# Optimization experiments

Hardware: AMD Instinct MI355X
Metric: run time of the kernel (lower is better)

Reference implementation:

```python
import jax, jax.numpy as jnp
import numpy as np

NB, H, C, HID, EMB = 4, 12, 1024, 768, 512
E, M, L, SPAN = 22, 4, 16, 32
TD, INTER = 20, 256
NN = E + E * M + L
NREL, NLAYERS = 3, 4

def _build_adj():
    # static relational adjacency: r0 entity<->its mentions, r1 mention<->co-entity mention, r2 mention<->link
    A = np.zeros((NREL, NN, NN), np.float32)
    for e in range(E):
        for m in range(M):
            mi = E + e * M + m
            A[0, e, mi] = A[0, mi, e] = 1.0
            for m2 in range(M):
                if m2 != m:
                    A[1, mi, E + e * M + m2] = 1.0
            li = E + E * M + ((e * M + m) % L)
            A[2, mi, li] = A[2, li, mi] = 1.0
    A = A / (A.sum(-1, keepdims=True) + 1e-5)
    return jnp.asarray(A)

_ADJ = _build_adj()
_TYPES = np.concatenate([np.zeros(E, np.int32), np.ones(E * M, np.int32), np.full(L, 2, np.int32)])

def _forward(sequence_output, attention, W_trans, b_trans, type_embed,
             rgcn_Wrel0, rgcn_Wself0, rgcn_Wrel, rgcn_Wself,
             fs_w1, fs_b1, fs_g1, fs_be1, fs_w2, fs_b2, fs_g2, fs_be2,
             fc_w1, fc_b1, fc_g1, fc_be1, fc_w2, fc_b2, fc_g2, fc_be2,
             cr_w1, cr_b1, cr_w2, cr_b2, cr_w3, cr_b3,
             mention_idx, link_start):
    n = sequence_output.shape[0]
    b = jnp.arange(n)[:, None, None]
    seq = sequence_output @ W_trans + b_trans            # [n,C,EMB] extractor_trans
    attq = attention.transpose(0, 2, 1, 3)               # [n,C,H,C] query-major
    # --- make_graph: mention / entity nodes (gather + logsumexp pooling) ---
    m_rep = seq[b, mention_idx]                          # [n,E,M,EMB]
    m_att = attq[b, mention_idx]                         # [n,E,M,H,C]
    e_rep = jax.nn.logsumexp(m_rep, axis=2)              # [n,E,EMB]
    e_att = m_att.mean(axis=2)                           # [n,E,H,C]
    # --- link nodes: attention-weighted span pooling ---
    idx = link_start[:, :, None] + jnp.arange(SPAN)      # [n,L,SPAN]
    span = seq[b, idx]                                   # [n,L,SPAN,EMB]
    att_rows = attq[b, idx]                              # [n,L,SPAN,H,C]
    col_idx = jnp.broadcast_to(idx[:, :, None, None, :], (n, L, SPAN, H, SPAN))
    block = jnp.take_along_axis(att_rows, col_idx, axis=4).mean(axis=3)  # [n,L,SPAN,SPAN]
    link_rep = jnp.einsum('nlst,nltd->nld', block, span) / SPAN          # [n,L,EMB]
    # --- node matrix + type embedding ---
    nodes = jnp.concatenate([e_rep, m_rep.reshape(n, E * M, EMB), link_rep], axis=1)
    tfeat = jnp.broadcast_to(type_embed[_TYPES][None], (n, NN, TD))
    h = jnp.concatenate([nodes, tfeat], axis=-1)         # [n,NN,EMB+TD]
    # --- RGCN ---
    def rgcn_layer(hh, Wrel, Wself):
        msg = jnp.einsum('rij,njd,rdo->nio', _ADJ, hh, Wrel)
        return jax.nn.relu(msg + hh @ Wself)
    h = rgcn_layer(h, rgcn_Wrel0, rgcn_Wself0)
    for l in range(NLAYERS - 1):
        h = rgcn_layer(h, rgcn_Wrel[l], rgcn_Wself[l])
    # --- relation_map: structure + attention-weighted context ---
    entity_stru = h[:, :E]                               # [n,E,EMB]
    ea = e_att.mean(axis=2)                              # [n,E,C]
    ea = ea / (ea.sum(-1, keepdims=True) + 1e-5)
    e_ctx = jnp.einsum('nec,ncd->ned', ea, seq)          # [n,E,EMB]
    ec = entity_stru + e_ctx
    fmap = (ec[:, :, None, :] * ec[:, None, :, :]).transpose(0, 3, 1, 2)  # [n,EMB,E,E]
    # --- SE fusion (fusion_s / fusion_c, BN in eval form) ---
    conv1x1 = lambda x, w, bb: jnp.einsum('nchw,oc->nohw', x, w) + bb[None, :, None, None]
    bn = lambda x, g, be: x * g[None, :, None, None] + be[None, :, None, None]
    s = bn(conv1x1(jax.nn.relu(bn(conv1x1(fmap, fs_w1, fs_b1), fs_g1, fs_be1)), fs_w2, fs_b2), fs_g2, fs_be2)
    pooled = fmap.mean(axis=(2, 3), keepdims=True)
    cb = bn(conv1x1(jax.nn.relu(bn(conv1x1(pooled, fc_w1, fc_b1), fc_g1, fc_be1)), fc_w2, fc_b2), fc_g2, fc_be2)
    fused = fmap * jax.nn.sigmoid(s + cb)
    # --- conv_reason 5x5 blocks ---
    dn = ('NCHW', 'OIHW', 'NCHW')
    conv = lambda x, w, bb: jax.lax.conv_general_dilated(x, w, (1, 1), 'SAME', dimension_numbers=dn) + bb[None, :, None, None]
    r = jax.nn.relu(conv(fused, cr_w1, cr_b1))
    r = jax.nn.relu(conv(r, cr_w2, cr_b2))
    return jax.nn.relu(conv(r, cr_w3, cr_b3))            # [n,EMB,E,E]

def setup_inputs():
    key = jax.random.key(0)
    ks = jax.random.split(key, 24)
    p = lambda k, sh: jax.random.normal(k, sh, jnp.float32) * 0.02
    z = lambda sh: jnp.zeros(sh, jnp.float32)
    o = lambda sh: jnp.ones(sh, jnp.float32)
    return {
        'sequence_output': jax.random.normal(ks[0], (NB, C, HID), jnp.float32),
        'attention': jax.random.uniform(ks[1], (NB, H, C, C), jnp.float32),
        'W_trans': p(ks[2], (HID, EMB)), 'b_trans': z((EMB,)),
        'type_embed': p(ks[3], (3, TD)),
        'rgcn_Wrel0': p(ks[4], (NREL, EMB + TD, EMB)), 'rgcn_Wself0': p(ks[5], (EMB + TD, EMB)),
        'rgcn_Wrel': p(ks[6], (NLAYERS - 1, NREL, EMB, EMB)), 'rgcn_Wself': p(ks[7], (NLAYERS - 1, EMB, EMB)),
        'fs_w1': p(ks[8], (INTER, EMB)), 'fs_b1': z((INTER,)), 'fs_g1': o((INTER,)), 'fs_be1': z((INTER,)),
        'fs_w2': p(ks[9], (EMB, INTER)), 'fs_b2': z((EMB,)), 'fs_g2': o((EMB,)), 'fs_be2': z((EMB,)),
        'fc_w1': p(ks[10], (INTER, EMB)), 'fc_b1': z((INTER,)), 'fc_g1': o((INTER,)), 'fc_be1': z((INTER,)),
        'fc_w2': p(ks[11], (EMB, INTER)), 'fc_b2': z((EMB,)), 'fc_g2': o((EMB,)), 'fc_be2': z((EMB,)),
        'cr_w1': p(ks[12], (INTER, EMB, 5, 5)), 'cr_b1': z((INTER,)),
        'cr_w2': p(ks[13], (INTER, INTER, 5, 5)), 'cr_b2': z((INTER,)),
        'cr_w3': p(ks[14], (EMB, INTER, 5, 5)), 'cr_b3': z((EMB,)),
        'mention_idx': jax.random.randint(ks[15], (NB, E, M), 0, C),
        'link_start': jnp.sort(jax.random.randint(ks[16], (NB, L), 0, C - SPAN), axis=-1),
    }

def reference(sequence_output, attention, W_trans, b_trans, type_embed,
              rgcn_Wrel0, rgcn_Wself0, rgcn_Wrel, rgcn_Wself,
              fs_w1, fs_b1, fs_g1, fs_be1, fs_w2, fs_b2, fs_g2, fs_be2,
              fc_w1, fc_b1, fc_g1, fc_be1, fc_w2, fc_b2, fc_g2, fc_be2,
              cr_w1, cr_b1, cr_w2, cr_b2, cr_w3, cr_b3,
              mention_idx, link_start):
    return _forward(sequence_output, attention, W_trans, b_trans, type_embed,
                    rgcn_Wrel0, rgcn_Wself0, rgcn_Wrel, rgcn_Wself,
                    fs_w1, fs_b1, fs_g1, fs_be1, fs_w2, fs_b2, fs_g2, fs_be2,
                    fc_w1, fc_b1, fc_g1, fc_be1, fc_w2, fc_b2, fc_g2, fc_be2,
                    cr_w1, cr_b1, cr_w2, cr_b2, cr_w3, cr_b3,
                    mention_idx, link_start)
```

## Files before the change

### kernel.cpp

```cpp
#include <hip/hip_runtime.h>
#include <hip/hip_bf16.h>
#include <stdint.h>

typedef long long ll;
typedef float f32x4 __attribute__((ext_vector_type(4)));
typedef __bf16 bf16x8 __attribute__((ext_vector_type(8)));
typedef __bf16 bf16x4 __attribute__((ext_vector_type(4)));

__global__ void k_castT_split(const float* __restrict__ in, __bf16* __restrict__ hi,
                              __bf16* __restrict__ lo, int R, int C){
  ll idx = (ll)blockIdx.x*256 + threadIdx.x;
  if (idx >= (ll)R*C) return;
  int r = (int)(idx % R); int c = (int)(idx / R);
  float x = in[(ll)r*C + c];
  __bf16 h = (__bf16)x;
  hi[idx] = h; lo[idx] = (__bf16)(x - (float)h);
}

__global__ void k_wcatT2(const float* __restrict__ Wrel, const float* __restrict__ Wself,
                         __bf16* __restrict__ hi, __bf16* __restrict__ lo,
                         int Din, int Kpad){
  __shared__ float t[32][33];
  int l = blockIdx.z;
  const float* wr = Wrel + (ll)l*3*Din*512;
  const float* ws2 = Wself + (ll)l*Din*512;
  __bf16* hb = hi + (ll)l*512*Kpad;
  __bf16* lb = lo + (ll)l*512*Kpad;
  int k0 = blockIdx.x*32, o0 = blockIdx.y*32;
  int tx = threadIdx.x, ty = threadIdx.y;
  for (int j=ty; j<32; j+=8){
    int k = k0 + j; float v = 0.f;
    if (k < 3*Din) v = wr[(ll)k*512 + o0+tx];
    else if (k < 4*Din) v = ws2[(ll)(k-3*Din)*512 + o0+tx];
    t[j][tx] = v;
  }
  __syncthreads();
  for (int j=ty; j<32; j+=8){
    float x = t[tx][j];
    __bf16 h = (__bf16)x;
    hb[(ll)(o0+j)*Kpad + k0+tx] = h;
    lb[(ll)(o0+j)*Kpad + k0+tx] = (__bf16)(x - (float)h);
  }
}

__global__ void k_seqT(const float* __restrict__ seq, __bf16* __restrict__ hi,
                       __bf16* __restrict__ lo){
  __shared__ float t[32][33];
  int n = blockIdx.z;
  int r0 = blockIdx.x*32, c0 = blockIdx.y*32;
  int tx = threadIdx.x, ty = threadIdx.y;
  for (int j=ty; j<32; j+=8)
    t[j][tx] = seq[((ll)n*1024 + r0+j)*512 + c0+tx];
  __syncthreads();
  for (int j=ty; j<32; j+=8){
    float x = t[tx][j];
    __bf16 h = (__bf16)x;
    ll o = ((ll)n*512 + c0+j)*1024 + r0+tx;
    hi[o] = h; lo[o] = (__bf16)(x - (float)h);
  }
}

__global__ void wt_make_all(const float* __restrict__ w1, const float* __restrict__ w2,
                            const float* __restrict__ w3, __bf16* __restrict__ d1,
                            __bf16* __restrict__ d2, __bf16* __restrict__ d3){
  int b = blockIdx.x;
  const float* w; __bf16* dst; int C, o;
  if (b < 256){ w=w1; dst=d1; C=512; o=b; }
  else if (b < 512){ w=w2; dst=d2; C=256; o=b-256; }
  else { w=w3; dst=d3; C=256; o=b-512; }
  for (int c=threadIdx.x; c<C; c+=256){
    const float* src = w + ((size_t)o*C + c)*25;
    float v[25];
    #pragma unroll
    for (int t=0;t<25;t++) v[t] = src[t];
    #pragma unroll
    for (int t=0;t<25;t++) dst[((size_t)o*25 + t)*C + c] = (__bf16)v[t];
  }
}

template<int SPLIT, int MODE, int BN>
__global__ __launch_bounds__(512) void gemm_mfma(
    const float* __restrict__ A,
    const __bf16* __restrict__ Bhi, const __bf16* __restrict__ Blo,
    float* __restrict__ Cf, __bf16* __restrict__ Cb,
    int M, int N, int K, ll sA, ll sB, ll sC,
    const float* __restrict__ biasN, const float* __restrict__ biasM,
    const float* __restrict__ gM, const float* __restrict__ beM,
    const __bf16* __restrict__ Fm, const float* __restrict__ CBV)
{
  constexpr int NF = BN/32;
  constexpr int SL = (4096 + BN*64) * (SPLIT?2:1);
  constexpr int REDB = 256*2*NF*16;
  constexpr int LDSB = (2*SL > REDB) ? 2*SL : REDB;
  __shared__ char lds[LDSB];

  int b = blockIdx.z;
  A += sA*b; Bhi += sB*b; if (SPLIT) Blo += sB*b;

  const int tid = threadIdx.x;
  const int slice = tid>>8;
  const int tl = tid & 255;
  const int w4 = (tid>>6)&3;
  const int grp = tid>>8;
  const int l15 = tid&15, lg=(tid&63)>>4, lg16=lg*16;
  const int wave_m0=(w4>>1)*32, wave_n0=(w4&1)*(BN/2);
  const int m0 = blockIdx.y*64, n0 = blockIdx.x*BN;

  char* sA_H = lds + slice*SL;
  char* sB_H = sA_H + 4096;
  char* sA_L = sB_H + BN*64;
  char* sB_L = sA_L + 4096;

  const int sa_row=tl>>2, sa_c8=tl&3;
  const int sa_byte = sa_row*64 + ((sa_c8*16) ^ (((sa_row>>1)&3)<<4));
  const int gmA = m0 + sa_row;

  int baseA[2], baseB[NF];
  #pragma unroll
  for (int mf=0; mf<2; ++mf){
    int r = wave_m0 + mf*16 + l15;
    baseA[mf] = r*64 + (lg16 ^ (((r>>1)&3)<<4));
  }
  #pragma unroll
  for (int nf=0; nf<NF; ++nf){
    int r = wave_n0 + nf*16 + l15;
    baseB[nf] = r*64 + (lg16 ^ (((r>>1)&3)<<4));
  }

  f32x4 acc[2][NF] = {};

  for (int k0=0; k0<K; k0+=64){
    int kk = k0 + slice*32;
    __syncthreads();
    {
      float f[8] = {0,0,0,0,0,0,0,0};
      if (gmA < M){
        float4 p0 = *reinterpret_cast<const float4*>(A + (ll)gmA*K + kk + sa_c8*8);
        float4 p1 = *reinterpret_cast<const float4*>(A + (ll)gmA*K + kk + sa_c8*8 + 4);
        f[0]=p0.x; f[1]=p0.y; f[2]=p0.z; f[3]=p0.w;
        f[4]=p1.x; f[5]=p1.y; f[6]=p1.z; f[7]=p1.w;
      }
      bf16x8 h, l;
      #pragma unroll
      for (int j=0;j<8;j++){
        h[j] = (__bf16)f[j];
        if (SPLIT) l[j] = (__bf16)(f[j] - (float)h[j]);
      }
      *reinterpret_cast<bf16x8*>(sA_H + sa_byte) = h;
      if (SPLIT) *reinterpret_cast<bf16x8*>(sA_L + sa_byte) = l;
    }
    #pragma unroll
    for (int i=0;i<BN/64;i++){
      int idx = tl + i*256;
      int row = idx>>2, c8 = idx&3;
      int gn = n0 + row;
      int byte = row*64 + ((c8*16) ^ (((row>>1)&3)<<4));
      bf16x8 v = {};
      if (gn < N) v = *reinterpret_cast<const bf16x8*>(Bhi + (ll)gn*K + kk + c8*8);
      *reinterpret_cast<bf16x8*>(sB_H + byte) = v;
      if (SPLIT){
        bf16x8 vl = {};
        if (gn < N) vl = *reinterpret_cast<const bf16x8*>(Blo + (ll)gn*K + kk + c8*8);
        *reinterpret_cast<bf16x8*>(sB_L + byte) = vl;
      }
    }
    __syncthreads();
    bf16x8 aH[2], bH[NF];
    #pragma unroll
    for (int mf=0; mf<2; ++mf) aH[mf] = *reinterpret_cast<const bf16x8*>(sA_H + baseA[mf]);
    #pragma unroll
    for (int nf=0; nf<NF; ++nf) bH[nf] = *reinterpret_cast<const bf16x8*>(sB_H + baseB[nf]);
    if (SPLIT){
      bf16x8 aL[2], bL[NF];
      #pragma unroll
      for (int mf=0; mf<2; ++mf) aL[mf] = *reinterpret_cast<const bf16x8*>(sA_L + baseA[mf]);
      #pragma unroll
      for (int nf=0; nf<NF; ++nf) bL[nf] = *reinterpret_cast<const bf16x8*>(sB_L + baseB[nf]);
      #pragma unroll
      for (int mf=0; mf<2; ++mf)
        #pragma unroll
        for (int nf=0; nf<NF; ++nf){
          acc[mf][nf] = __builtin_amdgcn_mfma_f32_16x16x32_bf16(aH[mf], bH[nf], acc[mf][nf], 0,0,0);
          acc[mf][nf] = __builtin_amdgcn_mfma_f32_16x16x32_bf16(aH[mf], bL[nf], acc[mf][nf], 0,0,0);
          acc[mf][nf] = __builtin_amdgcn_mfma_f32_16x16x32_bf16(aL[mf], bH[nf], acc[mf][nf], 0,0,0);
        }
    } else {
      #pragma unroll
      for (int mf=0; mf<2; ++mf)
        #pragma unroll
        for (int nf=0; nf<NF; ++nf)
          acc[mf][nf] = __builtin_amdgcn_mfma_f32_16x16x32_bf16(aH[mf], bH[nf], acc[mf][nf], 0,0,0);
    }
  }

  __syncthreads();
  if (grp==1){
    char* rp = lds + (ll)(tid-256)*(2*NF*16);
    #pragma unroll
    for (int mf=0; mf<2; ++mf)
      #pragma unroll
      for (int nf=0; nf<NF; ++nf)
        *reinterpret_cast<f32x4*>(rp + (mf*NF+nf)*16) = acc[mf][nf];
  }
  __syncthreads();
  if (grp!=0) return;
  {
    char* rp = lds + (ll)tid*(2*NF*16);
    #pragma unroll
    for (int mf=0; mf<2; ++mf)
      #pragma unroll
      for (int nf=0; nf<NF; ++nf)
        acc[mf][nf] += *reinterpret_cast<f32x4*>(rp + (mf*NF+nf)*16);
  }

  if (MODE==0 || MODE==1){
    float* C = Cf + sC*b;
    #pragma unroll
    for (int mf=0; mf<2; ++mf){
      int gmb = m0 + wave_m0 + mf*16 + lg*4;
      #pragma unroll
      for (int nf=0; nf<NF; ++nf){
        int gn = n0 + wave_n0 + nf*16 + l15;
        if (gn >= N) continue;
        float bn_ = (MODE==0 && biasN) ? biasN[gn] : 0.f;
        f32x4 a = acc[mf][nf];
        #pragma unroll
        for (int r=0;r<4;r++){
          int gm = gmb + r;
          if (gm < M){
            float v = a[r] + bn_;
            if (MODE==1) v = fmaxf(v, 0.f);
            C[(ll)gm*N + gn] = v;
          }
        }
      }
    }
  } else if (MODE==2){
    __bf16* C = Cb + sC*b;
    #pragma unroll
    for (int mf=0; mf<2; ++mf){
      int gmb = m0 + wave_m0 + mf*16 + lg*4;
      float b0=biasM[gmb], b1=biasM[gmb+1], b2=biasM[gmb+2], b3=biasM[gmb+3];
      float g0=gM[gmb], g1=gM[gmb+1], g2=gM[gmb+2], g3=gM[gmb+3];
      float e0=beM[gmb], e1=beM[gmb+1], e2=beM[gmb+2], e3=beM[gmb+3];
      #pragma unroll
      for (int nf=0; nf<NF; ++nf){
        int gn = n0 + wave_n0 + nf*16 + l15;
        if (gn >= N) continue;
        f32x4 a = acc[mf][nf];
        union { bf16x4 v; uint2 u; } pk;
        pk.v[0] = (__bf16)fmaxf((a[0]+b0)*g0+e0, 0.f);
        pk.v[1] = (__bf16)fmaxf((a[1]+b1)*g1+e1, 0.f);
        pk.v[2] = (__bf16)fmaxf((a[2]+b2)*g2+e2, 0.f);
        pk.v[3] = (__bf16)fmaxf((a[3]+b3)*g3+e3, 0.f);
        *reinterpret_cast<uint2*>(C + (ll)gn*M + gmb) = pk.u;
      }
    }
  } else {
    __bf16* C = Cb + sC*b;
    const __bf16* fm = Fm + (ll)b*484*512;
    const float* cb = CBV + (ll)b*512;
    #pragma unroll
    for (int mf=0; mf<2; ++mf){
      int gmb = m0 + wave_m0 + mf*16 + lg*4;
      float b0=biasM[gmb], b1=biasM[gmb+1], b2=biasM[gmb+2], b3=biasM[gmb+3];
      float g0=gM[gmb], g1=gM[gmb+1], g2=gM[gmb+2], g3=gM[gmb+3];
      float e0=beM[gmb], e1=beM[gmb+1], e2=beM[gmb+2], e3=beM[gmb+3];
      float c0=cb[gmb], c1=cb[gmb+1], c2=cb[gmb+2], c3=cb[gmb+3];
      #pragma unroll
      for (int nf=0; nf<NF; ++nf){
        int gn = n0 + wave_n0 + nf*16 + l15;
        if (gn >= N) continue;
        f32x4 a = acc[mf][nf];
        bf16x4 fmv = *reinterpret_cast<const bf16x4*>(fm + (ll)gn*512 + gmb);
        float s0 = (a[0]+b0)*g0+e0 + c0;
        float s1 = (a[1]+b1)*g1+e1 + c1;
        float s2 = (a[2]+b2)*g2+e2 + c2;
        float s3 = (a[3]+b3)*g3+e3 + c3;
        union { bf16x4 v; uint2 u; } pk;
        pk.v[0] = (__bf16)((float)fmv[0] / (1.f + expf(-s0)));
        pk.v[1] = (__bf16)((float)fmv[1] / (1.f + expf(-s1)));
        pk.v[2] = (__bf16)((float)fmv[2] / (1.f + expf(-s2)));
        pk.v[3] = (__bf16)((float)fmv[3] / (1.f + expf(-s3)));
        int py = gn/22, px = gn%22;
        int e = (py+2)*32 + px + 2;
        *reinterpret_cast<uint2*>(C + (ll)e*512 + gmb) = pk.u;
      }
    }
  }
}

template<int CIN, int OCHT, bool FINAL>
__global__ __launch_bounds__(256) void conv5_mfma(
    const __bf16* __restrict__ Xg, const __bf16* __restrict__ Wt,
    const float* __restrict__ bias, __bf16* __restrict__ Xout,
    float* __restrict__ outF)
{
  __shared__ bf16x8 Xs8[272*32/8];
  __shared__ bf16x8 Ws8[5*64*32/8];
  char* xs = (char*)Xs8;
  char* wsm = (char*)Ws8;

  const int tid = threadIdx.x;
  const int l = tid & 63;
  const int l15 = l & 15, lg = l >> 4, lg16 = (l>>4)*16;
  const int w = tid >> 6;
  const int wave_o0 = (w>>1)*32;
  const int wave_p0 = (w&1)*64;
  const int b = blockIdx.z;
  const int p0 = blockIdx.x*128;
  const int o0 = blockIdx.y*64;

  int orow0 = wave_o0 + l15;
  int orow1 = wave_o0 + 16 + l15;
  int baseA0 = orow0*64 + (lg16 ^ (((orow0>>1)&3)<<4));
  int baseA1 = orow1*64 + (lg16 ^ (((orow1>>1)&3)<<4));
  int pl[4];
  #pragma unroll
  for (int pf=0; pf<4; ++pf) pl[pf] = wave_p0 + pf*16 + l15;

  f32x4 acc[2][4] = {};

  const int NCB = CIN/32;
  for (int cblk=0; cblk<NCB; ++cblk){
    __syncthreads();
    #pragma unroll
    for (int i=0;i<5;i++){
      int idx = tid + i*256;
      if (idx < 1088){
        int e = idx>>2, c8 = idx&3;
        const __bf16* g = Xg + ((size_t)(b*928 + p0 + e))*CIN + cblk*32 + c8*8;
        bf16x8 v = *reinterpret_cast<const bf16x8*>(g);
        int byte = e*64 + ((c8*16) ^ (((e>>1)&3)<<4));
        *reinterpret_cast<bf16x8*>(xs + byte) = v;
      }
    }
    for (int g5=0; g5<5; ++g5){
      if (g5>0) __syncthreads();
      #pragma unroll
      for (int i=0;i<5;i++){
        int idx = tid + i*256;
        int tapL = idx>>8, r = idx&255;
        int o = r>>2, c8 = r&3;
        const __bf16* g = Wt + ((size_t)(o0+o)*25 + (g5*5+tapL))*CIN + cblk*32 + c8*8;
        bf16x8 v = *reinterpret_cast<const bf16x8*>(g);
        int byte = tapL*4096 + o*64 + ((c8*16) ^ (((o>>1)&3)<<4));
        *reinterpret_cast<bf16x8*>(wsm + byte) = v;
      }
      __syncthreads();
      #pragma unroll
      for (int tapL=0; tapL<5; ++tapL){
        bf16x8 a0 = *reinterpret_cast<const bf16x8*>(wsm + tapL*4096 + baseA0);
        bf16x8 a1 = *reinterpret_cast<const bf16x8*>(wsm + tapL*4096 + baseA1);
        int koff = g5*32 + tapL;
        #pragma unroll
        for (int pf=0; pf<4; ++pf){
          int e = pl[pf] + koff;
          bf16x8 bv = *reinterpret_cast<const bf16x8*>(xs + e*64 + (lg16 ^ (((e>>1)&3)<<4)));
          acc[0][pf] = __builtin_amdgcn_mfma_f32_16x16x32_bf16(a0, bv, acc[0][pf], 0,0,0);
          acc[1][pf] = __builtin_amdgcn_mfma_f32_16x16x32_bf16(a1, bv, acc[1][pf], 0,0,0);
        }
      }
    }
  }

  #pragma unroll
  for (int of=0; of<2; ++of){
    int og = o0 + wave_o0 + of*16 + lg*4;
    float b0 = bias[og], b1 = bias[og+1], b2 = bias[og+2], b3 = bias[og+3];
    #pragma unroll
    for (int pf=0; pf<4; ++pf){
      int p = p0 + pl[pf];
      int py = p>>5, px = p&31;
      if (py>=22 || px>=22) continue;
      f32x4 a = acc[of][pf];
      float v0 = fmaxf(a[0]+b0, 0.f), v1 = fmaxf(a[1]+b1, 0.f);
      float v2 = fmaxf(a[2]+b2, 0.f), v3 = fmaxf(a[3]+b3, 0.f);
      if (FINAL){
        size_t base = ((size_t)b*OCHT + og)*484 + py*22 + px;
        outF[base] = v0; outF[base+484] = v1; outF[base+968] = v2; outF[base+1452] = v3;
      } else {
        union { bf16x4 v; uint2 u; } pk;
        pk.v[0] = (__bf16)v0; pk.v[1] = (__bf16)v1; pk.v[2] = (__bf16)v2; pk.v[3] = (__bf16)v3;
        int e = p + 66;
        *reinterpret_cast<uint2*>(Xout + ((size_t)(b*928 + e))*OCHT + og) = pk.u;
      }
    }
  }
}

__global__ void k_nodes(const float* __restrict__ seq, const float* __restrict__ att,
                        const int* __restrict__ midx, const int* __restrict__ ls_,
                        const float* __restrict__ te, float* __restrict__ h0){
  __shared__ float part[32][8];
  __shared__ float wv[32];
  int b = blockIdx.x;
  if (b < 88){
    int n = b/22, e = b%22;
    int rows[4];
    #pragma unroll
    for (int m=0;m<4;m++) rows[m] = midx[(n*22+e)*4+m];
    for (int d=threadIdx.x; d<512; d+=256){
      float v[4]; float mx = -1e30f;
      #pragma unroll
      for (int m=0;m<4;m++){
        v[m] = seq[((ll)n*1024+rows[m])*512 + d];
        h0[((ll)n*126+22+e*4+m)*532 + d] = v[m];
        mx = fmaxf(mx, v[m]);
      }
      float s = 0.f;
      #pragma unroll
      for (int m=0;m<4;m++) s += expf(v[m]-mx);
      h0[((ll)n*126+e)*532 + d] = mx + logf(s);
    }
  } else if (b < 152){
    int bb = b-88;
    int n = bb/16, l = bb%16;
    int ls = ls_[n*16+l];
    int t = threadIdx.x; int tt = t>>3, lane = t&7;
    float acc = 0.f;
    for (int i=lane; i<384; i+=8){
      int h = i>>5, s = i&31;
      acc += att[((ll)(n*12+h)*1024 + ls+s)*1024 + (ls+tt)];
    }
    part[tt][lane] = acc; __syncthreads();
    if (lane==0){
      float s2=0.f;
      #pragma unroll
      for (int q=0;q<8;q++) s2 += part[tt][q];
      wv[tt] = s2*(1.f/12.f);
    }
    __syncthreads();
    for (int d=t; d<512; d+=256){
      float a2 = 0.f;
      for (int tk=0;tk<32;tk++) a2 += wv[tk]*seq[((ll)n*1024+ls+tk)*512 + d];
      h0[((ll)n*126+110+l)*532 + d] = a2*(1.f/32.f);
    }
  } else {
    int idx = (b-152)*256 + threadIdx.x;
    if (idx < 4*126*20){
      int t = idx%20; int i = (idx/20)%126; int n = idx/(20*126);
      int ty = (i<22)?0:((i<110)?1:2);
      h0[((ll)n*126+i)*532 + 512 + t] = te[ty*20+t];
    }
  }
}

__global__ void k_ea(const float* __restrict__ att, const int* __restrict__ midx, float* __restrict__ ea){
  int n = blockIdx.x/22, e = blockIdx.x%22;
  int t = threadIdx.x;
  __shared__ float vals[1024];
  __shared__ float red[256];
  int rows[4];
  #pragma unroll
  for (int m=0;m<4;m++) rows[m] = midx[(n*22+e)*4+m];
  float local = 0.f;
  for (int c=t; c<1024; c+=256){
    float acc = 0.f;
    #pragma unroll
    for (int m=0;m<4;m++){
      const float* base = att + ((ll)n*12*1024 + rows[m])*1024 + c;
      for (int h=0;h<12;h++) acc += base[(ll)h*1024*1024];
    }
    acc *= (1.f/48.f);
    vals[c] = acc; local += acc;
  }
  red[t] = local; __syncthreads();
  for (int s=128;s>0;s>>=1){ if (t<s) red[t]+=red[t+s]; __syncthreads(); }
  float denom = red[0] + 1e-5f;
  for (int c=t; c<1024; c+=256) ea[((ll)n*22+e)*1024 + c] = vals[c]/denom;
}

__global__ void k_buildX_s(const float* __restrict__ h, float* __restrict__ X,
                           int Din, int ldX){
  int n = blockIdx.x/126, i = blockIdx.x%126;
  const float* hb = h + (ll)n*126*Din;
  ll rowoff = (ll)(n*126+i)*ldX;
  const float inv1 = 1.f/(1.f+1e-5f), inv3 = 1.f/(3.f+1e-5f), inv4 = 1.f/(4.f+1e-5f);
  for (int d=threadIdx.x; d<Din; d+=256){
    float m0v=0.f, m1v=0.f, m2v=0.f;
    if (i < 22){
      int base = 22 + i*4;
      float s = hb[(ll)(base+0)*Din+d] + hb[(ll)(base+1)*Din+d]
              + hb[(ll)(base+2)*Din+d] + hb[(ll)(base+3)*Din+d];
      m0v = s * inv4;
    } else if (i < 110){
      int em = i-22, e = em>>2, base = 22+(e<<2);
      m0v = hb[(ll)e*Din+d] * inv1;
      float s1 = 0.f;
      #pragma unroll
      for (int m2=0;m2<4;m2++) if (base+m2 != i) s1 += hb[(ll)(base+m2)*Din+d];
      m1v = s1 * inv3;
      m2v = hb[(ll)(110+(em&15))*Din+d] * inv1;
    } else {
      int li0 = i-110;
      int cnt = (li0<8)?6:5;
      float s = 0.f;
      for (int t2=0;t2<cnt;t2++) s += hb[(ll)(22+li0+16*t2)*Din+d];
      m2v = s / ((float)cnt + 1e-5f);
    }
    float hh = hb[(ll)i*Din+d];
    X[rowoff + 0*Din + d] = m0v;
    X[rowoff + 1*Din + d] = m1v;
    X[rowoff + 2*Din + d] = m2v;
    X[rowoff + 3*Din + d] = hh;
  }
  for (int k=4*Din+threadIdx.x; k<ldX; k+=256) X[rowoff + k] = 0.f;
}

__global__ void k_ec(const float* __restrict__ hfin, const float* __restrict__ ectx, float* __restrict__ ec){
  int idx = blockIdx.x*256 + threadIdx.x;
  int d = idx & 511; int e = (idx>>9)%22; int n = idx/(22*512);
  ec[idx] = hfin[((ll)n*126+e)*512 + d] + ectx[idx];
}

__global__ void k_fmapT(const float* __restrict__ ec, __bf16* __restrict__ fmapT){
  int idx = blockIdx.x*256 + threadIdx.x;
  int ch = idx & 511; int p = (idx>>9) % 484; int n = idx/(484*512);
  int i = p/22, j = p%22;
  float v = ec[((ll)n*22+i)*512+ch] * ec[((ll)n*22+j)*512+ch];
  fmapT[idx] = (__bf16)v;
}

__global__ void k_poolcb(const float* __restrict__ ec,
                         const float* __restrict__ w1, const float* __restrict__ b1,
                         const float* __restrict__ g1, const float* __restrict__ be1,
                         const float* __restrict__ w2, const float* __restrict__ b2,
                         const float* __restrict__ g2, const float* __restrict__ be2,
                         float* __restrict__ cb){
  int n = blockIdx.x; int t = threadIdx.x;
  __shared__ float ps[512], t1[256];
  for (int c=t; c<512; c+=256){
    float s = 0.f;
    for (int i=0;i<22;i++) s += ec[((ll)n*22+i)*512 + c];
    ps[c] = s*s*(1.f/484.f);
  }
  __syncthreads();
  {
    float acc = 0.f;
    for (int c=0;c<512;c++) acc += w1[t*512+c]*ps[c];
    float v = g1[t]*(acc+b1[t]) + be1[t];
    t1[t] = fmaxf(v, 0.f);
  }
  __syncthreads();
  for (int o=t; o<512; o+=256){
    float acc = 0.f;
    for (int c=0;c<256;c++) acc += w2[o*256+c]*t1[c];
    cb[n*512+o] = g2[o]*(acc+b2[o]) + be2[o];
  }
}

extern "C" void kernel_launch(void* const* d_in, const int* in_sizes, int n_in,
                              void* d_out, int out_size, void* d_ws, size_t ws_size,
                              hipStream_t stream)
{
  (void)in_sizes; (void)n_in; (void)out_size; (void)ws_size;
  const float* seqout   = (const float*)d_in[0];
  const float* att      = (const float*)d_in[1];
  const float* W_trans  = (const float*)d_in[2];
  const float* b_trans  = (const float*)d_in[3];
  const float* type_emb = (const float*)d_in[4];
  const float* Wrel0    = (const float*)d_in[5];
  const float* Wself0   = (const float*)d_in[6];
  const float* Wrel     = (const float*)d_in[7];
  const float* Wself    = (const float*)d_in[8];
  const float* fs_w1    = (const float*)d_in[9];
  const float* fs_b1    = (const float*)d_in[10];
  const float* fs_g1    = (const float*)d_in[11];
  const float* fs_be1   = (const float*)d_in[12];
  const float* fs_w2    = (const float*)d_in[13];
  const float* fs_b2    = (const float*)d_in[14];
  const float* fs_g2    = (const float*)d_in[15];
  const float* fs_be2   = (const float*)d_in[16];
  const float* fc_w1    = (const float*)d_in[17];
  const float* fc_b1    = (const float*)d_in[18];
  const float* fc_g1    = (const float*)d_in[19];
  const float* fc_be1   = (const float*)d_in[20];
  const float* fc_w2    = (const float*)d_in[21];
  const float* fc_b2    = (const float*)d_in[22];
  const float* fc_g2    = (const float*)d_in[23];
  const float* fc_be2   = (const float*)d_in[24];
  const float* cr_w1    = (const float*)d_in[25];
  const float* cr_b1    = (const float*)d_in[26];
  const float* cr_w2    = (const float*)d_in[27];
  const float* cr_b2    = (const float*)d_in[28];
  const float* cr_w3    = (const float*)d_in[29];
  const float* cr_b3    = (const float*)d_in[30];
  const int*   midx     = (const int*)d_in[31];
  const int*   lstart   = (const int*)d_in[32];
  float* out            = (float*)d_out;

  char* wsb = (char*)d_ws;
  size_t off = 0;
  auto allocB = [&](size_t nbytes)->char*{ char* p = wsb + off; off += (nbytes + 63) & ~(size_t)63; return p; };
  float* seq   = (float*)allocB((size_t)4096*512*4);
  float* h0    = (float*)allocB((size_t)504*532*4);
  float* ea    = (float*)allocB((size_t)88*1024*4);
  float* ectx  = (float*)allocB((size_t)88*512*4);
  float* X     = (float*)allocB((size_t)504*2176*4);
  float* hA    = (float*)allocB((size_t)504*512*4);
  float* hB    = (float*)allocB((size_t)504*512*4);
  float* ec    = (float*)allocB((size_t)88*512*4);
  float* cbv   = (float*)allocB(2048*4);
  __bf16* wth  = (__bf16*)allocB((size_t)512*768*2);
  __bf16* wtl  = (__bf16*)allocB((size_t)512*768*2);
  __bf16* sqTh = (__bf16*)allocB((size_t)4*512*1024*2);
  __bf16* sqTl = (__bf16*)allocB((size_t)4*512*1024*2);
  __bf16* wc0h = (__bf16*)allocB((size_t)512*2176*2);
  __bf16* wc0l = (__bf16*)allocB((size_t)512*2176*2);
  __bf16* wc13h= (__bf16*)allocB((size_t)3*512*2048*2);
  __bf16* wc13l= (__bf16*)allocB((size_t)3*512*2048*2);
  __bf16* fmapT= (__bf16*)allocB((size_t)4*484*512*2);
  __bf16* s1bT = (__bf16*)allocB((size_t)4*484*256*2);
  __bf16* Xint1 = (__bf16*)allocB((size_t)4*928*512*2);
  __bf16* Xint2 = (__bf16*)allocB((size_t)4*928*256*2);
  __bf16* Xint3 = (__bf16*)allocB((size_t)4*928*256*2);
  __bf16* Wt1   = (__bf16*)allocB((size_t)256*25*512*2);
  __bf16* Wt2   = (__bf16*)allocB((size_t)256*25*256*2);
  __bf16* Wt3   = (__bf16*)allocB((size_t)512*25*256*2);

  (void)hipMemsetAsync(Xint1, 0, (size_t)(4*928*512 + 4*928*256 + 4*928*256)*2, stream);

  wt_make_all<<<1024,256,0,stream>>>(cr_w1, cr_w2, cr_w3, Wt1, Wt2, Wt3);
  k_castT_split<<<1536,256,0,stream>>>(W_trans, wth, wtl, 768, 512);
  k_wcatT2<<<dim3(68,16,1),dim3(32,8),0,stream>>>(Wrel0, Wself0, wc0h, wc0l, 532, 2176);
  k_wcatT2<<<dim3(64,16,3),dim3(32,8),0,stream>>>(Wrel, Wself, wc13h, wc13l, 512, 2048);

  gemm_mfma<1,0,128><<<dim3(4,64,1),512,0,stream>>>(seqout, wth, wtl, seq, nullptr,
      4096,512,768, 0,0,0, b_trans,nullptr,nullptr,nullptr, nullptr,nullptr);
  k_nodes<<<192,256,0,stream>>>(seq, att, midx, lstart, type_emb, h0);
  k_ea<<<88,256,0,stream>>>(att, midx, ea);
  k_seqT<<<dim3(32,16,4),dim3(32,8),0,stream>>>(seq, sqTh, sqTl);
  gemm_mfma<1,0,64><<<dim3(8,1,4),512,0,stream>>>(ea, sqTh, sqTl, ectx, nullptr,
      22,512,1024, (ll)22*1024, (ll)512*1024, (ll)22*512,
      nullptr,nullptr,nullptr,nullptr, nullptr,nullptr);
  k_buildX_s<<<504,256,0,stream>>>(h0, X, 532, 2176);
  gemm_mfma<1,1,64><<<dim3(8,8,1),512,0,stream>>>(X, wc0h, wc0l, hA, nullptr,
      504,512,2176, 0,0,0, nullptr,nullptr,nullptr,nullptr, nullptr,nullptr);
  float* hcur = hA; float* hnxt = hB;
  for (int l=0;l<3;l++){
    k_buildX_s<<<504,256,0,stream>>>(hcur, X, 512, 2048);
    gemm_mfma<1,1,64><<<dim3(8,8,1),512,0,stream>>>(X,
        wc13h + (ll)l*512*2048, wc13l + (ll)l*512*2048, hnxt, nullptr,
        504,512,2048, 0,0,0, nullptr,nullptr,nullptr,nullptr, nullptr,nullptr);
    float* t = hcur; hcur = hnxt; hnxt = t;
  }
  k_ec<<<176,256,0,stream>>>(hcur, ectx, ec);
  k_fmapT<<<3872,256,0,stream>>>(ec, fmapT);
  gemm_mfma<0,2,64><<<dim3(8,4,4),512,0,stream>>>(fs_w1, fmapT, nullptr, nullptr, s1bT,
      256,484,512, 0, (ll)484*512, (ll)484*256,
      nullptr, fs_b1, fs_g1, fs_be1, nullptr,nullptr);
  k_poolcb<<<4,256,0,stream>>>(ec, fc_w1, fc_b1, fc_g1, fc_be1,
                               fc_w2, fc_b2, fc_g2, fc_be2, cbv);
  gemm_mfma<0,4,64><<<dim3(8,8,4),512,0,stream>>>(fs_w2, s1bT, nullptr, nullptr, Xint1,
      512,484,256, 0, (ll)484*256, (ll)928*512,
      nullptr, fs_b2, fs_g2, fs_be2, fmapT, cbv);
  conv5_mfma<512,256,false><<<dim3(6,4,4),256,0,stream>>>(Xint1, Wt1, cr_b1, Xint2, nullptr);
  conv5_mfma<256,256,false><<<dim3(6,4,4),256,0,stream>>>(Xint2, Wt2, cr_b2, Xint3, nullptr);
  conv5_mfma<256,512,true ><<<dim3(6,8,4),256,0,stream>>>(Xint3, Wt3, cr_b3, nullptr, out);
}
```

Baseline: 554.2 us.

## Merge prep and gather kernels, fold ec into fmap, stream conv weights from global

Several small launches are merged into single grid-partitioned kernels: all weight casts and transposes into k_prep, node gather, ea and seq transpose into k_gather, and ec, fmapT and pooled context-bias into k_fmap2. The ec add is recomputed inline, so that intermediate buffer and its pass go away. Separately, conv5_mfma no longer stages weights in LDS. Each lane loads its A fragments directly from global memory with a one-tap prefetch, which removes the per-group barriers but adds uncached-style global loads inside the MFMA loop.

```diff
diff --git a/kernel.cpp b/kernel.cpp
--- a/kernel.cpp
+++ b/kernel.cpp
@@ -7,74 +7,64 @@
 typedef __bf16 bf16x8 __attribute__((ext_vector_type(8)));
 typedef __bf16 bf16x4 __attribute__((ext_vector_type(4)));
 
-__global__ void k_castT_split(const float* __restrict__ in, __bf16* __restrict__ hi,
-                              __bf16* __restrict__ lo, int R, int C){
-  ll idx = (ll)blockIdx.x*256 + threadIdx.x;
-  if (idx >= (ll)R*C) return;
-  int r = (int)(idx % R); int c = (int)(idx / R);
-  float x = in[(ll)r*C + c];
-  __bf16 h = (__bf16)x;
-  hi[idx] = h; lo[idx] = (__bf16)(x - (float)h);
-}
-
-__global__ void k_wcatT2(const float* __restrict__ Wrel, const float* __restrict__ Wself,
-                         __bf16* __restrict__ hi, __bf16* __restrict__ lo,
-                         int Din, int Kpad){
+__global__ void k_prep(const float* __restrict__ cr_w1, const float* __restrict__ cr_w2,
+                       const float* __restrict__ cr_w3, __bf16* __restrict__ Wt1,
+                       __bf16* __restrict__ Wt2, __bf16* __restrict__ Wt3,
+                       const float* __restrict__ W_trans, __bf16* __restrict__ wth,
+                       __bf16* __restrict__ wtl,
+                       const float* __restrict__ Wrel0, const float* __restrict__ Wself0,
+                       __bf16* __restrict__ wc0h, __bf16* __restrict__ wc0l,
+                       const float* __restrict__ Wrel, const float* __restrict__ Wself,
+                       __bf16* __restrict__ wc13h, __bf16* __restrict__ wc13l)
+{
   __shared__ float t[32][33];
-  int l = blockIdx.z;
-  const float* wr = Wrel + (ll)l*3*Din*512;
-  const float* ws2 = Wself + (ll)l*Din*512;
-  __bf16* hb = hi + (ll)l*512*Kpad;
-  __bf16* lb = lo + (ll)l*512*Kpad;
-  int k0 = blockIdx.x*32, o0 = blockIdx.y*32;
-  int tx = threadIdx.x, ty = threadIdx.y;
-  for (int j=ty; j<32; j+=8){
-    int k = k0 + j; float v = 0.f;
-    if (k < 3*Din) v = wr[(ll)k*512 + o0+tx];
-    else if (k < 4*Din) v = ws2[(ll)(k-3*Din)*512 + o0+tx];
-    t[j][tx] = v;
-  }
-  __syncthreads();
-  for (int j=ty; j<32; j+=8){
-    float x = t[tx][j];
+  int b = blockIdx.x; int tid = threadIdx.x;
+  if (b < 1024){
+    const float* w; __bf16* dst; int C, o;
+    if (b < 256){ w=cr_w1; dst=Wt1; C=512; o=b; }
+    else if (b < 512){ w=cr_w2; dst=Wt2; C=256; o=b-256; }
+    else { w=cr_w3; dst=Wt3; C=256; o=b-512; }
+    for (int c=tid; c<C; c+=256){
+      const float* src = w + ((size_t)o*C + c)*25;
+      float v[25];
+      #pragma unroll
+      for (int q=0;q<25;q++) v[q] = src[q];
+      #pragma unroll
+      for (int q=0;q<25;q++) dst[((size_t)o*25 + q)*C + c] = (__bf16)v[q];
+    }
+  } else if (b < 2560){
+    ll idx = (ll)(b-1024)*256 + tid;
+    int r = (int)(idx % 768); int c = (int)(idx / 768);
+    float x = W_trans[(ll)r*512 + c];
     __bf16 h = (__bf16)x;
-    hb[(ll)(o0+j)*Kpad + k0+tx] = h;
-    lb[(ll)(o0+j)*Kpad + k0+tx] = (__bf16)(x - (float)h);
-  }
-}
-
-__global__ void k_seqT(const float* __restrict__ seq, __bf16* __restrict__ hi,
-                       __bf16* __restrict__ lo){
-  __shared__ float t[32][33];
-  int n = blockIdx.z;
-  int r0 = blockIdx.x*32, c0 = blockIdx.y*32;
-  int tx = threadIdx.x, ty = threadIdx.y;
-  for (int j=ty; j<32; j+=8)
-    t[j][tx] = seq[((ll)n*1024 + r0+j)*512 + c0+tx];
-  __syncthreads();
-  for (int j=ty; j<32; j+=8){
-    float x = t[tx][j];
-    __bf16 h = (__bf16)x;
-    ll o = ((ll)n*512 + c0+j)*1024 + r0+tx;
-    hi[o] = h; lo[o] = (__bf16)(x - (float)h);
-  }
-}
-
-__global__ void wt_make_all(const float* __restrict__ w1, const float* __restrict__ w2,
-                            const float* __restrict__ w3, __bf16* __restrict__ d1,
-                            __bf16* __restrict__ d2, __bf16* __restrict__ d3){
-  int b = blockIdx.x;
-  const float* w; __bf16* dst; int C, o;
-  if (b < 256){ w=w1; dst=d1; C=512; o=b; }
-  else if (b < 512){ w=w2; dst=d2; C=256; o=b-256; }
-  else { w=w3; dst=d3; C=256; o=b-512; }
-  for (int c=threadIdx.x; c<C; c+=256){
-    const float* src = w + ((size_t)o*C + c)*25;
-    float v[25];
-    #pragma unroll
-    for (int t=0;t<25;t++) v[t] = src[t];
-    #pragma unroll
-    for (int t=0;t<25;t++) dst[((size_t)o*25 + t)*C + c] = (__bf16)v[t];
+    wth[idx] = h; wtl[idx] = (__bf16)(x - (float)h);
+  } else {
+    int Din, Kpad, bx, by;
+    const float* wr; const float* ws2; __bf16* hb; __bf16* lb;
+    if (b < 3648){
+      int b2 = b-2560; bx = b2 % 68; by = b2/68; Din=532; Kpad=2176;
+      wr = Wrel0; ws2 = Wself0; hb = wc0h; lb = wc0l;
+    } else {
+      int b3 = b-3648; int l = b3/1024; int r2 = b3%1024; bx = r2%64; by = r2/64;
+      Din=512; Kpad=2048;
+      wr = Wrel + (ll)l*3*512*512; ws2 = Wself + (ll)l*512*512;
+      hb = wc13h + (ll)l*512*2048; lb = wc13l + (ll)l*512*2048;
+    }
+    int k0 = bx*32, o0 = by*32;
+    int tx = tid&31, ty = tid>>5;
+    for (int j=ty; j<32; j+=8){
+      int k = k0 + j; float v = 0.f;
+      if (k < 3*Din) v = wr[(ll)k*512 + o0+tx];
+      else if (k < 4*Din) v = ws2[(ll)(k-3*Din)*512 + o0+tx];
+      t[j][tx] = v;
+    }
+    __syncthreads();
+    for (int j=ty; j<32; j+=8){
+      float x = t[tx][j];
+      __bf16 h = (__bf16)x;
+      hb[(ll)(o0+j)*Kpad + k0+tx] = h;
+      lb[(ll)(o0+j)*Kpad + k0+tx] = (__bf16)(x - (float)h);
+    }
   }
 }
 
@@ -297,9 +287,7 @@
     float* __restrict__ outF)
 {
   __shared__ bf16x8 Xs8[272*32/8];
-  __shared__ bf16x8 Ws8[5*64*32/8];
   char* xs = (char*)Xs8;
-  char* wsm = (char*)Ws8;
 
   const int tid = threadIdx.x;
   const int l = tid & 63;
@@ -311,10 +299,9 @@
   const int p0 = blockIdx.x*128;
   const int o0 = blockIdx.y*64;
 
-  int orow0 = wave_o0 + l15;
-  int orow1 = wave_o0 + 16 + l15;
-  int baseA0 = orow0*64 + (lg16 ^ (((orow0>>1)&3)<<4));
-  int baseA1 = orow1*64 + (lg16 ^ (((orow1>>1)&3)<<4));
+  const __bf16* wbase0 = Wt + ((size_t)(o0+wave_o0+l15)*25)*CIN + lg*8;
+  const __bf16* wbase1 = Wt + ((size_t)(o0+wave_o0+16+l15)*25)*CIN + lg*8;
+
   int pl[4];
   #pragma unroll
   for (int pf=0; pf<4; ++pf) pl[pf] = wave_p0 + pf*16 + l15;
@@ -335,31 +322,25 @@
         *reinterpret_cast<bf16x8*>(xs + byte) = v;
       }
     }
-    for (int g5=0; g5<5; ++g5){
-      if (g5>0) __syncthreads();
-      #pragma unroll
-      for (int i=0;i<5;i++){
-        int idx = tid + i*256;
-        int tapL = idx>>8, r = idx&255;
-        int o = r>>2, c8 = r&3;
-        const __bf16* g = Wt + ((size_t)(o0+o)*25 + (g5*5+tapL))*CIN + cblk*32 + c8*8;
-        bf16x8 v = *reinterpret_cast<const bf16x8*>(g);
-        int byte = tapL*4096 + o*64 + ((c8*16) ^ (((o>>1)&3)<<4));
-        *reinterpret_cast<bf16x8*>(wsm + byte) = v;
-      }
-      __syncthreads();
-      #pragma unroll
-      for (int tapL=0; tapL<5; ++tapL){
-        bf16x8 a0 = *reinterpret_cast<const bf16x8*>(wsm + tapL*4096 + baseA0);
-        bf16x8 a1 = *reinterpret_cast<const bf16x8*>(wsm + tapL*4096 + baseA1);
-        int koff = g5*32 + tapL;
-        #pragma unroll
-        for (int pf=0; pf<4; ++pf){
-          int e = pl[pf] + koff;
-          bf16x8 bv = *reinterpret_cast<const bf16x8*>(xs + e*64 + (lg16 ^ (((e>>1)&3)<<4)));
-          acc[0][pf] = __builtin_amdgcn_mfma_f32_16x16x32_bf16(a0, bv, acc[0][pf], 0,0,0);
-          acc[1][pf] = __builtin_amdgcn_mfma_f32_16x16x32_bf16(a1, bv, acc[1][pf], 0,0,0);
-        }
+    __syncthreads();
+    const __bf16* w0 = wbase0 + cblk*32;
+    const __bf16* w1 = wbase1 + cblk*32;
+    bf16x8 a0n = *reinterpret_cast<const bf16x8*>(w0);
+    bf16x8 a1n = *reinterpret_cast<const bf16x8*>(w1);
+    #pragma unroll
+    for (int tap=0; tap<25; ++tap){
+      bf16x8 a0 = a0n, a1 = a1n;
+      if (tap < 24){
+        a0n = *reinterpret_cast<const bf16x8*>(w0 + (size_t)(tap+1)*CIN);
+        a1n = *reinterpret_cast<const bf16x8*>(w1 + (size_t)(tap+1)*CIN);
+      }
+      int koff = (tap/5)*32 + (tap%5);
+      #pragma unroll
+      for (int pf=0; pf<4; ++pf){
+        int e = pl[pf] + koff;
+        bf16x8 bv = *reinterpret_cast<const bf16x8*>(xs + e*64 + (lg16 ^ (((e>>1)&3)<<4)));
+        acc[0][pf] = __builtin_amdgcn_mfma_f32_16x16x32_bf16(a0, bv, acc[0][pf], 0,0,0);
+        acc[1][pf] = __builtin_amdgcn_mfma_f32_16x16x32_bf16(a1, bv, acc[1][pf], 0,0,0);
       }
     }
   }
@@ -389,18 +370,24 @@
   }
 }
 
-__global__ void k_nodes(const float* __restrict__ seq, const float* __restrict__ att,
-                        const int* __restrict__ midx, const int* __restrict__ ls_,
-                        const float* __restrict__ te, float* __restrict__ h0){
+__global__ void k_gather(const float* __restrict__ seq, const float* __restrict__ att,
+                         const int* __restrict__ midx, const int* __restrict__ ls_,
+                         const float* __restrict__ te, float* __restrict__ h0,
+                         float* __restrict__ ea, __bf16* __restrict__ sqTh,
+                         __bf16* __restrict__ sqTl)
+{
   __shared__ float part[32][8];
   __shared__ float wv[32];
-  int b = blockIdx.x;
+  __shared__ float vals[1024];
+  __shared__ float red[256];
+  __shared__ float tt2[32][33];
+  int b = blockIdx.x; int t = threadIdx.x;
   if (b < 88){
     int n = b/22, e = b%22;
     int rows[4];
     #pragma unroll
     for (int m=0;m<4;m++) rows[m] = midx[(n*22+e)*4+m];
-    for (int d=threadIdx.x; d<512; d+=256){
+    for (int d=t; d<512; d+=256){
       float v[4]; float mx = -1e30f;
       #pragma unroll
       for (int m=0;m<4;m++){
@@ -417,7 +404,7 @@
     int bb = b-88;
     int n = bb/16, l = bb%16;
     int ls = ls_[n*16+l];
-    int t = threadIdx.x; int tt = t>>3, lane = t&7;
+    int tt = t>>3, lane = t&7;
     float acc = 0.f;
     for (int i=lane; i<384; i+=8){
       int h = i>>5, s = i&31;
@@ -436,39 +423,50 @@
       for (int tk=0;tk<32;tk++) a2 += wv[tk]*seq[((ll)n*1024+ls+tk)*512 + d];
       h0[((ll)n*126+110+l)*532 + d] = a2*(1.f/32.f);
     }
+  } else if (b < 192){
+    int idx = (b-152)*256 + t;
+    if (idx < 4*126*20){
+      int q = idx%20; int i = (idx/20)%126; int n = idx/(20*126);
+      int ty = (i<22)?0:((i<110)?1:2);
+      h0[((ll)n*126+i)*532 + 512 + q] = te[ty*20+q];
+    }
+  } else if (b < 280){
+    int bb = b-192;
+    int n = bb/22, e = bb%22;
+    int rows[4];
+    #pragma unroll
+    for (int m=0;m<4;m++) rows[m] = midx[(n*22+e)*4+m];
+    float local = 0.f;
+    for (int c=t; c<1024; c+=256){
+      float acc = 0.f;
+      #pragma unroll
+      for (int m=0;m<4;m++){
+        const float* base = att + ((ll)n*12*1024 + rows[m])*1024 + c;
+        #pragma unroll
+        for (int h=0;h<12;h++) acc += base[(ll)h*1048576];
+      }
+      acc *= (1.f/48.f);
+      vals[c] = acc; local += acc;
+    }
+    red[t] = local; __syncthreads();
+    for (int s=128;s>0;s>>=1){ if (t<s) red[t]+=red[t+s]; __syncthreads(); }
+    float denom = red[0] + 1e-5f;
+    for (int c=t; c<1024; c+=256) ea[((ll)bb)*1024 + c] = vals[c]/denom;
   } else {
-    int idx = (b-152)*256 + threadIdx.x;
-    if (idx < 4*126*20){
-      int t = idx%20; int i = (idx/20)%126; int n = idx/(20*126);
-      int ty = (i<22)?0:((i<110)?1:2);
-      h0[((ll)n*126+i)*532 + 512 + t] = te[ty*20+t];
-    }
-  }
-}
-
-__global__ void k_ea(const float* __restrict__ att, const int* __restrict__ midx, float* __restrict__ ea){
-  int n = blockIdx.x/22, e = blockIdx.x%22;
-  int t = threadIdx.x;
-  __shared__ float vals[1024];
-  __shared__ float red[256];
-  int rows[4];
-  #pragma unroll
-  for (int m=0;m<4;m++) rows[m] = midx[(n*22+e)*4+m];
-  float local = 0.f;
-  for (int c=t; c<1024; c+=256){
-    float acc = 0.f;
-    #pragma unroll
-    for (int m=0;m<4;m++){
-      const float* base = att + ((ll)n*12*1024 + rows[m])*1024 + c;
-      for (int h=0;h<12;h++) acc += base[(ll)h*1024*1024];
-    }
-    acc *= (1.f/48.f);
-    vals[c] = acc; local += acc;
-  }
-  red[t] = local; __syncthreads();
-  for (int s=128;s>0;s>>=1){ if (t<s) red[t]+=red[t+s]; __syncthreads(); }
-  float denom = red[0] + 1e-5f;
-  for (int c=t; c<1024; c+=256) ea[((ll)n*22+e)*1024 + c] = vals[c]/denom;
+    int b2 = b-280;
+    int n = b2>>9; int rem = b2&511;
+    int r0 = (rem&31)*32, c0 = (rem>>5)*32;
+    int tx = t&31, ty = t>>5;
+    for (int j=ty; j<32; j+=8)
+      tt2[j][tx] = seq[((ll)n*1024 + r0+j)*512 + c0+tx];
+    __syncthreads();
+    for (int j=ty; j<32; j+=8){
+      float x = tt2[tx][j];
+      __bf16 h = (__bf16)x;
+      ll o = ((ll)n*512 + c0+j)*1024 + r0+tx;
+      sqTh[o] = h; sqTl[o] = (__bf16)(x - (float)h);
+    }
+  }
 }
 
 __global__ void k_buildX_s(const float* __restrict__ h, float* __restrict__ X,
@@ -508,45 +506,43 @@
   for (int k=4*Din+threadIdx.x; k<ldX; k+=256) X[rowoff + k] = 0.f;
 }
 
-__global__ void k_ec(const float* __restrict__ hfin, const float* __restrict__ ectx, float* __restrict__ ec){
-  int idx = blockIdx.x*256 + threadIdx.x;
-  int d = idx & 511; int e = (idx>>9)%22; int n = idx/(22*512);
-  ec[idx] = hfin[((ll)n*126+e)*512 + d] + ectx[idx];
-}
-
-__global__ void k_fmapT(const float* __restrict__ ec, __bf16* __restrict__ fmapT){
-  int idx = blockIdx.x*256 + threadIdx.x;
-  int ch = idx & 511; int p = (idx>>9) % 484; int n = idx/(484*512);
-  int i = p/22, j = p%22;
-  float v = ec[((ll)n*22+i)*512+ch] * ec[((ll)n*22+j)*512+ch];
-  fmapT[idx] = (__bf16)v;
-}
-
-__global__ void k_poolcb(const float* __restrict__ ec,
-                         const float* __restrict__ w1, const float* __restrict__ b1,
-                         const float* __restrict__ g1, const float* __restrict__ be1,
-                         const float* __restrict__ w2, const float* __restrict__ b2,
-                         const float* __restrict__ g2, const float* __restrict__ be2,
-                         float* __restrict__ cb){
-  int n = blockIdx.x; int t = threadIdx.x;
+__global__ void k_fmap2(const float* __restrict__ hfin, const float* __restrict__ ectx,
+                        __bf16* __restrict__ fmapT,
+                        const float* __restrict__ w1, const float* __restrict__ b1,
+                        const float* __restrict__ g1, const float* __restrict__ be1,
+                        const float* __restrict__ w2, const float* __restrict__ b2,
+                        const float* __restrict__ g2, const float* __restrict__ be2,
+                        float* __restrict__ cb){
   __shared__ float ps[512], t1[256];
-  for (int c=t; c<512; c+=256){
-    float s = 0.f;
-    for (int i=0;i<22;i++) s += ec[((ll)n*22+i)*512 + c];
-    ps[c] = s*s*(1.f/484.f);
-  }
-  __syncthreads();
-  {
-    float acc = 0.f;
-    for (int c=0;c<512;c++) acc += w1[t*512+c]*ps[c];
-    float v = g1[t]*(acc+b1[t]) + be1[t];
-    t1[t] = fmaxf(v, 0.f);
-  }
-  __syncthreads();
-  for (int o=t; o<512; o+=256){
-    float acc = 0.f;
-    for (int c=0;c<256;c++) acc += w2[o*256+c]*t1[c];
-    cb[n*512+o] = g2[o]*(acc+b2[o]) + be2[o];
+  int b = blockIdx.x; int t = threadIdx.x;
+  if (b < 3872){
+    int idx = b*256 + t;
+    int ch = idx & 511; int p = (idx>>9) % 484; int n = idx/(484*512);
+    int i = p/22, j = p%22;
+    float vi = hfin[((ll)n*126+i)*512 + ch] + ectx[((ll)n*22+i)*512 + ch];
+    float vj = hfin[((ll)n*126+j)*512 + ch] + ectx[((ll)n*22+j)*512 + ch];
+    fmapT[idx] = (__bf16)(vi*vj);
+  } else {
+    int n = b-3872;
+    for (int c=t; c<512; c+=256){
+      float s = 0.f;
+      for (int i=0;i<22;i++)
+        s += hfin[((ll)n*126+i)*512 + c] + ectx[((ll)n*22+i)*512 + c];
+      ps[c] = s*s*(1.f/484.f);
+    }
+    __syncthreads();
+    {
+      float acc = 0.f;
+      for (int c=0;c<512;c++) acc += w1[t*512+c]*ps[c];
+      float v = g1[t]*(acc+b1[t]) + be1[t];
+      t1[t] = fmaxf(v, 0.f);
+    }
+    __syncthreads();
+    for (int o=t; o<512; o+=256){
+      float acc = 0.f;
+      for (int c=0;c<256;c++) acc += w2[o*256+c]*t1[c];
+      cb[n*512+o] = g2[o]*(acc+b2[o]) + be2[o];
+    }
   }
 }
 
@@ -600,7 +596,6 @@
   float* X     = (float*)allocB((size_t)504*2176*4);
   float* hA    = (float*)allocB((size_t)504*512*4);
   float* hB    = (float*)allocB((size_t)504*512*4);
-  float* ec    = (float*)allocB((size_t)88*512*4);
   float* cbv   = (float*)allocB(2048*4);
   __bf16* wth  = (__bf16*)allocB((size_t)512*768*2);
   __bf16* wtl  = (__bf16*)allocB((size_t)512*768*2);
@@ -621,16 +616,14 @@
 
   (void)hipMemsetAsync(Xint1, 0, (size_t)(4*928*512 + 4*928*256 + 4*928*256)*2, stream);
 
-  wt_make_all<<<1024,256,0,stream>>>(cr_w1, cr_w2, cr_w3, Wt1, Wt2, Wt3);
-  k_castT_split<<<1536,256,0,stream>>>(W_trans, wth, wtl, 768, 512);
-  k_wcatT2<<<dim3(68,16,1),dim3(32,8),0,stream>>>(Wrel0, Wself0, wc0h, wc0l, 532, 2176);
-  k_wcatT2<<<dim3(64,16,3),dim3(32,8),0,stream>>>(Wrel, Wself, wc13h, wc13l, 512, 2048);
+  k_prep<<<6720,256,0,stream>>>(cr_w1, cr_w2, cr_w3, Wt1, Wt2, Wt3,
+                                W_trans, wth, wtl,
+                                Wrel0, Wself0, wc0h, wc0l,
+                                Wrel, Wself, wc13h, wc13l);
 
   gemm_mfma<1,0,128><<<dim3(4,64,1),512,0,stream>>>(seqout, wth, wtl, seq, nullptr,
       4096,512,768, 0,0,0, b_trans,nullptr,nullptr,nullptr, nullptr,nullptr);
-  k_nodes<<<192,256,0,stream>>>(seq, att, midx, lstart, type_emb, h0);
-  k_ea<<<88,256,0,stream>>>(att, midx, ea);
-  k_seqT<<<dim3(32,16,4),dim3(32,8),0,stream>>>(seq, sqTh, sqTl);
+  k_gather<<<2328,256,0,stream>>>(seq, att, midx, lstart, type_emb, h0, ea, sqTh, sqTl);
   gemm_mfma<1,0,64><<<dim3(8,1,4),512,0,stream>>>(ea, sqTh, sqTl, ectx, nullptr,
       22,512,1024, (ll)22*1024, (ll)512*1024, (ll)22*512,
       nullptr,nullptr,nullptr,nullptr, nullptr,nullptr);
@@ -645,13 +638,12 @@
         504,512,2048, 0,0,0, nullptr,nullptr,nullptr,nullptr, nullptr,nullptr);
     float* t = hcur; hcur = hnxt; hnxt = t;
   }
-  k_ec<<<176,256,0,stream>>>(hcur, ectx, ec);
-  k_fmapT<<<3872,256,0,stream>>>(ec, fmapT);
+  k_fmap2<<<3876,256,0,stream>>>(hcur, ectx, fmapT,
+                                 fc_w1, fc_b1, fc_g1, fc_be1,
+                                 fc_w2, fc_b2, fc_g2, fc_be2, cbv);
   gemm_mfma<0,2,64><<<dim3(8,4,4),512,0,stream>>>(fs_w1, fmapT, nullptr, nullptr, s1bT,
       256,484,512, 0, (ll)484*512, (ll)484*256,
       nullptr, fs_b1, fs_g1, fs_be1, nullptr,nullptr);
-  k_poolcb<<<4,256,0,stream>>>(ec, fc_w1, fc_b1, fc_g1, fc_be1,
-                               fc_w2, fc_b2, fc_g2, fc_be2, cbv);
   gemm_mfma<0,4,64><<<dim3(8,8,4),512,0,stream>>>(fs_w2, s1bT, nullptr, nullptr, Xint1,
       512,484,256, 0, (ll)484*256, (ll)928*512,
       nullptr, fs_b2, fs_g2, fs_be2, fmapT, cbv);
```

New measurement: 631.5 us. 1.14x slower.
